# Kernel tuning notes

Measured on AMD Instinct MI355X. Metric: run time of the kernel, lower is better.

Reference implementation:

```python
import jax, jax.numpy as jnp
import numpy as np

N = 20000      # u/v nodes (dst == src, no block sampling)
E = 200000     # edges per direction
EIN = UIN = VIN = EOUT = 64
UOUT = VOUT = 128
NU = UOUT // 2
NV = VOUT // 2
ATT = VIN + EIN  # 128, W_ATTN output / concat dim


def _linear_params(key, din, dout):
    kw, kb = jax.random.split(key)
    s = 1.0 / np.sqrt(din)
    w = jax.random.uniform(kw, (din, dout), jnp.float32, -s, s)
    b = jax.random.uniform(kb, (dout,), jnp.float32, -s, s)
    return w, b


def setup_inputs() -> dict:
    key = jax.random.key(0)
    ks = jax.random.split(key, 20)
    inp = {
        "f_feat": jax.random.normal(ks[0], (E, EIN), jnp.float32),
        "b_feat": jax.random.normal(ks[1], (E, EIN), jnp.float32),
        "u_feat": jax.random.normal(ks[2], (N, UIN), jnp.float32),
        "v_feat": jax.random.normal(ks[3], (N, VIN), jnp.float32),
        "fw_src": jax.random.randint(ks[4], (E,), 0, N, jnp.int32),
        "fw_dst": jax.random.randint(ks[5], (E,), 0, N, jnp.int32),
        "bw_src": jax.random.randint(ks[6], (E,), 0, N, jnp.int32),
        "bw_dst": jax.random.randint(ks[7], (E,), 0, N, jnp.int32),
    }
    names_dims = [("e", EIN, EOUT), ("u", UIN, EOUT), ("v", VIN, EOUT),
                  ("au", UIN, ATT), ("av", VIN, ATT),
                  ("Wu", ATT, NU), ("Wv", ATT, NV),
                  ("Vu", UIN, UOUT - NU), ("Vv", VIN, VOUT - NV)]
    for i, (nm, di, do) in enumerate(names_dims):
        w, b = _linear_params(ks[8 + i], di, do)
        inp["w_" + nm] = w
        inp["b_" + nm] = b
    return inp


def _seg_softmax(x, seg, n):
    # softmax over edges grouped by destination node, per channel
    m = jax.ops.segment_max(x, seg, num_segments=n)       # [n, d]
    e = jnp.exp(x - m[seg])
    s = jax.ops.segment_sum(e, seg, num_segments=n)       # [n, d]
    return e / s[seg]


def reference(f_feat, b_feat, u_feat, v_feat, fw_src, fw_dst, bw_src, bw_dst,
              w_e, b_e, w_u, b_u, w_v, b_v, w_au, b_au, w_av, b_av,
              w_Wu, b_Wu, w_Wv, b_Wv, w_Vu, b_Vu, w_Vv, b_Vv):
    relu = jax.nn.relu
    src_he_u = u_feat @ w_u + b_u                 # [N, EOUT]
    src_he_v = v_feat @ w_v + b_v                 # [N, EOUT]
    dst_he_u = src_he_u                           # dst slice == full set
    dst_he_v = v_feat @ w_u + b_u                 # faithful: original applies u_linear to dst v feats
    fw_he_e = f_feat @ w_e + b_e                  # [E, EOUT]
    bw_he_e = b_feat @ w_e + b_e
    # edge updates (gather-add-activate)
    hf = relu(bw_he_e + dst_he_u[bw_src] + src_he_v[bw_dst])   # [E, EOUT]
    hb = relu(fw_he_e + src_he_u[fw_src] + dst_he_v[fw_dst])
    # per-edge concat features
    h_ve = jnp.concatenate([v_feat[bw_src], b_feat], -1)       # [E, ATT]
    h_ue = jnp.concatenate([u_feat[fw_src], f_feat], -1)       # [E, ATT]
    # attention scores: elementwise edge * gathered node projection
    h_att_u = u_feat @ w_au + b_au                # [N, ATT]
    h_att_v = v_feat @ w_av + b_av
    bw_edotv = h_ve * h_att_u[bw_src]
    fw_edotv = h_ue * h_att_v[fw_src]
    bw_sfm = _seg_softmax(bw_edotv, bw_dst, N)
    fw_sfm = _seg_softmax(fw_edotv, fw_dst, N)
    # weighted segment-sum aggregation
    agg_u = jax.ops.segment_sum(h_ve * bw_sfm, bw_dst, num_segments=N)  # [N, ATT]
    agg_v = jax.ops.segment_sum(h_ue * fw_sfm, fw_dst, num_segments=N)
    h_nu = relu(agg_u @ w_Wu + b_Wu)              # [N, NU]
    h_nv = relu(agg_v @ w_Wv + b_Wv)
    hu = jnp.concatenate([u_feat @ w_Vu + b_Vu, h_nu], -1)     # [N, UOUT]
    hv = jnp.concatenate([v_feat @ w_Vv + b_Vv, h_nv], -1)     # [N, VOUT]
    return (hf, hb, hu, hv)
```

## Files before the change

kernel.cpp:

```cpp
#include <hip/hip_runtime.h>

#define NNODES 20000
#define NEDGES 200000

__global__ __launch_bounds__(256)
void zero_kernel(float4* __restrict__ p, long n4)
{
    long i = (long)blockIdx.x * 256 + threadIdx.x;
    if (i < n4) p[i] = make_float4(0.f, 0.f, 0.f, 0.f);
}

__global__ __launch_bounds__(256)
void hist2_kernel(const int* __restrict__ dst0, const int* __restrict__ dst1,
                  int* __restrict__ deg0, int* __restrict__ deg1, int n)
{
    const int e = blockIdx.x * 256 + threadIdx.x;
    if (e >= n) return;
    if (blockIdx.y == 0) atomicAdd(&deg0[dst0[e]], 1);
    else                 atomicAdd(&deg1[dst1[e]], 1);
}

__global__ __launch_bounds__(1024)
void scan2_kernel(const int* __restrict__ deg0, const int* __restrict__ deg1,
                  int* __restrict__ rp0, int* __restrict__ rp1,
                  int* __restrict__ cur0, int* __restrict__ cur1, int n)
{
    const int* deg = blockIdx.x == 0 ? deg0 : deg1;
    int* rowptr    = blockIdx.x == 0 ? rp0  : rp1;
    int* cursor    = blockIdx.x == 0 ? cur0 : cur1;

    __shared__ int part[1024];
    const int t  = threadIdx.x;
    const int CH = (n + 1023) / 1024;
    const int base = t * CH;

    int s = 0;
    for (int i = 0; i < CH; ++i) {
        int idx = base + i;
        if (idx < n) s += deg[idx];
    }
    part[t] = s;
    __syncthreads();
    for (int off = 1; off < 1024; off <<= 1) {
        int v = 0;
        if (t >= off) v = part[t - off];
        __syncthreads();
        if (t >= off) part[t] += v;
        __syncthreads();
    }
    int run = (t == 0) ? 0 : part[t - 1];
    for (int i = 0; i < CH; ++i) {
        int idx = base + i;
        if (idx < n) {
            int dv = deg[idx];
            rowptr[idx] = run;
            cursor[idx] = run;
            run += dv;
        }
    }
    if (t == 1023) rowptr[n] = part[1023];
}

__global__ __launch_bounds__(256)
void scatter2_kernel(const int* __restrict__ dst0, const int* __restrict__ dst1,
                     int* __restrict__ cur0, int* __restrict__ cur1,
                     int* __restrict__ ei0, int* __restrict__ ei1, int n)
{
    const int e = blockIdx.x * 256 + threadIdx.x;
    if (e >= n) return;
    if (blockIdx.y == 0) { int p = atomicAdd(&cur0[dst0[e]], 1); ei0[p] = e; }
    else                 { int p = atomicAdd(&cur1[dst1[e]], 1); ei1[p] = e; }
}

__global__ __launch_bounds__(128)
void agg3_kernel(const float* __restrict__ fn0, const float* __restrict__ fe0,
                 const float* __restrict__ ha0, const int* __restrict__ src0,
                 const int* __restrict__ ei0,  const int* __restrict__ rp0,
                 float* __restrict__ agg0,
                 const float* __restrict__ fn1, const float* __restrict__ fe1,
                 const float* __restrict__ ha1, const int* __restrict__ src1,
                 const int* __restrict__ ei1,  const int* __restrict__ rp1,
                 float* __restrict__ agg1)
{
    const int y = blockIdx.y;
    const float* __restrict__ feat_node = y == 0 ? fn0 : fn1;
    const float* __restrict__ feat_edge = y == 0 ? fe0 : fe1;
    const float* __restrict__ h_att     = y == 0 ? ha0 : ha1;
    const int*   __restrict__ src       = y == 0 ? src0 : src1;
    const int*   __restrict__ eidx      = y == 0 ? ei0 : ei1;
    const int*   __restrict__ rowptr    = y == 0 ? rp0 : rp1;
    float*       __restrict__ agg       = y == 0 ? agg0 : agg1;

    const int d = blockIdx.x;
    const int c = threadIdx.x;
    const int lo = rowptr[d], hi = rowptr[d + 1];
    const bool low = c < 64;

    __shared__ int se[64];
    __shared__ int ss[64];

    float ssum = 0.f, anum = 0.f;

    for (int base = lo; base < hi; base += 64) {
        const int cnt = min(64, hi - base);
        if (c < cnt) {
            const int e = eidx[base + c];
            se[c] = e;
            ss[c] = src[e];
        }
        __syncthreads();

        int i = 0;
        for (; i + 4 <= cnt; i += 4) {
            float hv[4], at[4];
            #pragma unroll
            for (int j = 0; j < 4; ++j) {
                const int e = se[i + j];
                const int s = ss[i + j];
                hv[j] = low ? feat_node[(long)s * 64 + c]
                            : feat_edge[(long)e * 64 + (c - 64)];
                at[j] = h_att[(long)s * 128 + c];
            }
            #pragma unroll
            for (int j = 0; j < 4; ++j) {
                const float p = __expf(hv[j] * at[j]);
                ssum += p;
                anum += hv[j] * p;
            }
        }
        for (; i < cnt; ++i) {
            const int e = se[i];
            const int s = ss[i];
            const float hvv = low ? feat_node[(long)s * 64 + c]
                                  : feat_edge[(long)e * 64 + (c - 64)];
            const float att = h_att[(long)s * 128 + c];
            const float p = __expf(hvv * att);
            ssum += p;
            anum += hvv * p;
        }
        __syncthreads();
    }
    agg[(long)d * 128 + c] = (hi > lo) ? anum / ssum : 0.f;
}

struct LinArgs {
    const float* x[5];
    const float* W[5];
    const float* bias[5];
    float*       out[5];
    long         ostride[5];
};

template<int DIN, int DOUT, int BLOCK, bool RELU>
__global__ __launch_bounds__(BLOCK)
void lin_batch_kernel(LinArgs a, int nrows)
{
    constexpr int BR  = 16 * BLOCK / DOUT;
    constexpr int BRP = BR + 1;
    constexpr int KV  = DIN / 4;
    constexpr int JT  = DOUT / 4;

    const int y = blockIdx.y;
    const float* __restrict__ x    = a.x[y];
    const float* __restrict__ W    = a.W[y];
    const float* __restrict__ bias = a.bias[y];
    float* __restrict__ out        = a.out[y];
    const long ostride             = a.ostride[y];

    __shared__ float xs[DIN * BRP];
    __shared__ float Ws[DIN * DOUT];

    const int tid  = threadIdx.x;
    const int row0 = blockIdx.x * BR;

    for (int i = tid; i < DIN * DOUT / 4; i += BLOCK)
        ((float4*)Ws)[i] = ((const float4*)W)[i];

    const int kv = tid % KV;
    for (int rr = tid / KV; rr < BR; rr += BLOCK / KV) {
        const int row = row0 + rr;
        float4 v = make_float4(0.f, 0.f, 0.f, 0.f);
        if (row < nrows)
            v = ((const float4*)x)[(long)row * KV + kv];
        xs[(kv * 4 + 0) * BRP + rr] = v.x;
        xs[(kv * 4 + 1) * BRP + rr] = v.y;
        xs[(kv * 4 + 2) * BRP + rr] = v.z;
        xs[(kv * 4 + 3) * BRP + rr] = v.w;
    }
    __syncthreads();

    const int jt = tid % JT;
    const int rt = tid / JT;

    float4 b4 = ((const float4*)bias)[jt];
    float acc[4][4];
    #pragma unroll
    for (int r = 0; r < 4; ++r) {
        acc[r][0] = b4.x; acc[r][1] = b4.y; acc[r][2] = b4.z; acc[r][3] = b4.w;
    }

    #pragma unroll 8
    for (int k = 0; k < DIN; ++k) {
        float4 w = ((const float4*)(Ws + k * DOUT))[jt];
        float xr[4];
        #pragma unroll
        for (int r = 0; r < 4; ++r) xr[r] = xs[k * BRP + rt * 4 + r];
        #pragma unroll
        for (int r = 0; r < 4; ++r) {
            acc[r][0] = fmaf(xr[r], w.x, acc[r][0]);
            acc[r][1] = fmaf(xr[r], w.y, acc[r][1]);
            acc[r][2] = fmaf(xr[r], w.z, acc[r][2]);
            acc[r][3] = fmaf(xr[r], w.w, acc[r][3]);
        }
    }

    #pragma unroll
    for (int r = 0; r < 4; ++r) {
        const int row = row0 + rt * 4 + r;
        if (row >= nrows) continue;
        float4 o = make_float4(acc[r][0], acc[r][1], acc[r][2], acc[r][3]);
        if (RELU) {
            o.x = fmaxf(o.x, 0.f); o.y = fmaxf(o.y, 0.f);
            o.z = fmaxf(o.z, 0.f); o.w = fmaxf(o.w, 0.f);
        }
        *((float4*)(out + (long)row * ostride) + jt) = o;
    }
}

struct EdgeArgs {
    const float* x[2];
    const float* tabA[2];
    const float* tabB[2];
    const int*   idxA[2];
    const int*   idxB[2];
    float*       out[2];
};

__global__ __launch_bounds__(256)
void edge_batch_kernel(EdgeArgs a, const float* __restrict__ W,
                       const float* __restrict__ bias, int nrows)
{
    constexpr int DIN = 64, DOUT = 64, BLOCK = 256;
    constexpr int BR  = 16 * BLOCK / DOUT;
    constexpr int BRP = BR + 1;
    constexpr int KV  = DIN / 4;
    constexpr int JT  = DOUT / 4;

    const int y = blockIdx.y;
    const float* __restrict__ x    = a.x[y];
    const float* __restrict__ tabA = a.tabA[y];
    const float* __restrict__ tabB = a.tabB[y];
    const int* __restrict__ idxA   = a.idxA[y];
    const int* __restrict__ idxB   = a.idxB[y];
    float* __restrict__ out        = a.out[y];

    __shared__ float xs[DIN * BRP];
    __shared__ float Ws[DIN * DOUT];

    const int tid  = threadIdx.x;
    const int row0 = blockIdx.x * BR;

    for (int i = tid; i < DIN * DOUT / 4; i += BLOCK)
        ((float4*)Ws)[i] = ((const float4*)W)[i];

    const int kv = tid % KV;
    for (int rr = tid / KV; rr < BR; rr += BLOCK / KV) {
        const int row = row0 + rr;
        float4 v = make_float4(0.f, 0.f, 0.f, 0.f);
        if (row < nrows)
            v = ((const float4*)x)[(long)row * KV + kv];
        xs[(kv * 4 + 0) * BRP + rr] = v.x;
        xs[(kv * 4 + 1) * BRP + rr] = v.y;
        xs[(kv * 4 + 2) * BRP + rr] = v.z;
        xs[(kv * 4 + 3) * BRP + rr] = v.w;
    }
    __syncthreads();

    const int jt = tid % JT;
    const int rt = tid / JT;

    float4 b4 = ((const float4*)bias)[jt];
    float acc[4][4];
    #pragma unroll
    for (int r = 0; r < 4; ++r) {
        acc[r][0] = b4.x; acc[r][1] = b4.y; acc[r][2] = b4.z; acc[r][3] = b4.w;
    }

    #pragma unroll 8
    for (int k = 0; k < DIN; ++k) {
        float4 w = ((const float4*)(Ws + k * DOUT))[jt];
        float xr[4];
        #pragma unroll
        for (int r = 0; r < 4; ++r) xr[r] = xs[k * BRP + rt * 4 + r];
        #pragma unroll
        for (int r = 0; r < 4; ++r) {
            acc[r][0] = fmaf(xr[r], w.x, acc[r][0]);
            acc[r][1] = fmaf(xr[r], w.y, acc[r][1]);
            acc[r][2] = fmaf(xr[r], w.z, acc[r][2]);
            acc[r][3] = fmaf(xr[r], w.w, acc[r][3]);
        }
    }

    #pragma unroll
    for (int r = 0; r < 4; ++r) {
        const int row = row0 + rt * 4 + r;
        if (row >= nrows) continue;
        const int ia = idxA[row];
        const int ib = idxB[row];
        float4 ga = ((const float4*)(tabA + (long)ia * DOUT))[jt];
        float4 gb = ((const float4*)(tabB + (long)ib * DOUT))[jt];
        float4 o;
        o.x = fmaxf(acc[r][0] + ga.x + gb.x, 0.f);
        o.y = fmaxf(acc[r][1] + ga.y + gb.y, 0.f);
        o.z = fmaxf(acc[r][2] + ga.z + gb.z, 0.f);
        o.w = fmaxf(acc[r][3] + ga.w + gb.w, 0.f);
        *((float4*)(out + (long)row * DOUT) + jt) = o;
    }
}

extern "C" void kernel_launch(void* const* d_in, const int* in_sizes, int n_in,
                              void* d_out, int out_size, void* d_ws, size_t ws_size,
                              hipStream_t stream)
{
    const float* f_feat = (const float*)d_in[0];
    const float* b_feat = (const float*)d_in[1];
    const float* u_feat = (const float*)d_in[2];
    const float* v_feat = (const float*)d_in[3];
    const int* fw_src = (const int*)d_in[4];
    const int* fw_dst = (const int*)d_in[5];
    const int* bw_src = (const int*)d_in[6];
    const int* bw_dst = (const int*)d_in[7];
    const float* w_e  = (const float*)d_in[8];   const float* b_e  = (const float*)d_in[9];
    const float* w_u  = (const float*)d_in[10];  const float* b_u  = (const float*)d_in[11];
    const float* w_v  = (const float*)d_in[12];  const float* b_v  = (const float*)d_in[13];
    const float* w_au = (const float*)d_in[14];  const float* b_au = (const float*)d_in[15];
    const float* w_av = (const float*)d_in[16];  const float* b_av = (const float*)d_in[17];
    const float* w_Wu = (const float*)d_in[18];  const float* b_Wu = (const float*)d_in[19];
    const float* w_Wv = (const float*)d_in[20];  const float* b_Wv = (const float*)d_in[21];
    const float* w_Vu = (const float*)d_in[22];  const float* b_Vu = (const float*)d_in[23];
    const float* w_Vv = (const float*)d_in[24];  const float* b_Vv = (const float*)d_in[25];

    const int N = NNODES, E = NEDGES;

    float* out = (float*)d_out;
    float* hf = out;
    float* hb = hf + (long)E * 64;
    float* hu = hb + (long)E * 64;
    float* hv = hu + (long)N * 128;

    float* h_att_u = hf;
    float* h_att_v = h_att_u + (long)N * 128;

    float* ws = (float*)d_ws;
    float* src_he_u = ws;
    float* src_he_v = src_he_u + (long)N * 64;
    float* dst_he_v = src_he_v + (long)N * 64;
    float* agg_u    = dst_he_v + (long)N * 64;
    float* agg_v    = agg_u    + (long)N * 128;
    int*   ibase    = (int*)(agg_v + (long)N * 128);
    int* deg_b    = ibase;
    int* deg_f    = deg_b + N;
    int* rowptr_b = deg_f + N;
    int* rowptr_f = rowptr_b + (N + 1);
    int* cursor_b = rowptr_f + (N + 1);
    int* cursor_f = cursor_b + N;
    int* eidx_b   = cursor_f + N;
    int* eidx_f   = eidx_b + E;

    const size_t ws_need = (size_t)((long)8960000 + 520002 + 2) * sizeof(float);
    if (ws_size < ws_need) return;

    zero_kernel<<<dim3((2 * N / 4 + 255) / 256), dim3(256), 0, stream>>>(
        (float4*)deg_b, (long)2 * N / 4);

    const int gN64 = (N + 63) / 64;
    const int gN32 = (N + 31) / 32;
    const int gE64 = (E + 63) / 64;
    const int gE   = (E + 255) / 256;

    hist2_kernel<<<dim3(gE, 2), dim3(256), 0, stream>>>(
        bw_dst, fw_dst, deg_b, deg_f, E);
    scan2_kernel<<<dim3(2), dim3(1024), 0, stream>>>(
        deg_b, deg_f, rowptr_b, rowptr_f, cursor_b, cursor_f, N);
    scatter2_kernel<<<dim3(gE, 2), dim3(256), 0, stream>>>(
        bw_dst, fw_dst, cursor_b, cursor_f, eidx_b, eidx_f, E);

    {
        LinArgs a;
        a.x[0]=u_feat; a.W[0]=w_u;  a.bias[0]=b_u;  a.out[0]=src_he_u; a.ostride[0]=64;
        a.x[1]=v_feat; a.W[1]=w_v;  a.bias[1]=b_v;  a.out[1]=src_he_v; a.ostride[1]=64;
        a.x[2]=v_feat; a.W[2]=w_u;  a.bias[2]=b_u;  a.out[2]=dst_he_v; a.ostride[2]=64;
        a.x[3]=u_feat; a.W[3]=w_Vu; a.bias[3]=b_Vu; a.out[3]=hu;       a.ostride[3]=128;
        a.x[4]=v_feat; a.W[4]=w_Vv; a.bias[4]=b_Vv; a.out[4]=hv;       a.ostride[4]=128;
        lin_batch_kernel<64,64,256,false><<<dim3(gN64, 5), dim3(256), 0, stream>>>(a, N);
    }

    {
        LinArgs a = {};
        a.x[0]=u_feat; a.W[0]=w_au; a.bias[0]=b_au; a.out[0]=h_att_u; a.ostride[0]=128;
        a.x[1]=v_feat; a.W[1]=w_av; a.bias[1]=b_av; a.out[1]=h_att_v; a.ostride[1]=128;
        lin_batch_kernel<64,128,256,false><<<dim3(gN32, 2), dim3(256), 0, stream>>>(a, N);
    }

    agg3_kernel<<<dim3(N, 2), dim3(128), 0, stream>>>(
        v_feat, b_feat, h_att_u, bw_src, eidx_b, rowptr_b, agg_u,
        u_feat, f_feat, h_att_v, fw_src, eidx_f, rowptr_f, agg_v);

    {
        LinArgs a = {};
        a.x[0]=agg_u; a.W[0]=w_Wu; a.bias[0]=b_Wu; a.out[0]=hu + 64; a.ostride[0]=128;
        a.x[1]=agg_v; a.W[1]=w_Wv; a.bias[1]=b_Wv; a.out[1]=hv + 64; a.ostride[1]=128;
        lin_batch_kernel<128,64,128,true><<<dim3(gN32, 2), dim3(128), 0, stream>>>(a, N);
    }

    {
        EdgeArgs a;
        a.x[0]=b_feat; a.tabA[0]=src_he_u; a.tabB[0]=src_he_v;
        a.idxA[0]=bw_src; a.idxB[0]=bw_dst; a.out[0]=hf;
        a.x[1]=f_feat; a.tabA[1]=src_he_u; a.tabB[1]=dst_he_v;
        a.idxA[1]=fw_src; a.idxB[1]=fw_dst; a.out[1]=hb;
        edge_batch_kernel<<<dim3(gE64, 2), dim3(256), 0, stream>>>(a, w_e, b_e, E);
    }
}
```

Measured before the change: 476.8 us.

## Map one wavefront per destination node in attention aggregation with shuffles

Restructures the aggregation kernel so each 64-lane wavefront handles one destination node, with each lane covering two channels via float2 loads, and four nodes per 256-thread block. Edge and source indices are broadcast with wave shuffles instead of shared memory, which removes the per-chunk __syncthreads barriers. The aim is to cut synchronisation and block-scheduling overhead and to widen the memory accesses. In exchange each lane does twice the per-edge work, and node degree imbalance within a block can leave waves idle.

```diff
diff --git a/kernel.cpp b/kernel.cpp
--- a/kernel.cpp
+++ b/kernel.cpp
@@ -72,8 +72,8 @@
     else                 { int p = atomicAdd(&cur1[dst1[e]], 1); ei1[p] = e; }
 }
 
-__global__ __launch_bounds__(128)
-void agg3_kernel(const float* __restrict__ fn0, const float* __restrict__ fe0,
+__global__ __launch_bounds__(256)
+void agg4_kernel(const float* __restrict__ fn0, const float* __restrict__ fe0,
                  const float* __restrict__ ha0, const int* __restrict__ src0,
                  const int* __restrict__ ei0,  const int* __restrict__ rp0,
                  float* __restrict__ agg0,
@@ -91,56 +91,43 @@
     const int*   __restrict__ rowptr    = y == 0 ? rp0 : rp1;
     float*       __restrict__ agg       = y == 0 ? agg0 : agg1;
 
-    const int d = blockIdx.x;
-    const int c = threadIdx.x;
+    const int wave = threadIdx.x >> 6;
+    const int lane = threadIdx.x & 63;
+    const int d = blockIdx.x * 4 + wave;
+    if (d >= NNODES) return;
+
     const int lo = rowptr[d], hi = rowptr[d + 1];
-    const bool low = c < 64;
-
-    __shared__ int se[64];
-    __shared__ int ss[64];
-
-    float ssum = 0.f, anum = 0.f;
+    const int c2 = lane * 2;
+    const bool low = lane < 32;
+
+    float s0 = 0.f, s1 = 0.f, a0 = 0.f, a1 = 0.f;
 
     for (int base = lo; base < hi; base += 64) {
         const int cnt = min(64, hi - base);
-        if (c < cnt) {
-            const int e = eidx[base + c];
-            se[c] = e;
-            ss[c] = src[e];
-        }
-        __syncthreads();
-
-        int i = 0;
-        for (; i + 4 <= cnt; i += 4) {
-            float hv[4], at[4];
-            #pragma unroll
-            for (int j = 0; j < 4; ++j) {
-                const int e = se[i + j];
-                const int s = ss[i + j];
-                hv[j] = low ? feat_node[(long)s * 64 + c]
-                            : feat_edge[(long)e * 64 + (c - 64)];
-                at[j] = h_att[(long)s * 128 + c];
-            }
-            #pragma unroll
-            for (int j = 0; j < 4; ++j) {
-                const float p = __expf(hv[j] * at[j]);
-                ssum += p;
-                anum += hv[j] * p;
-            }
-        }
-        for (; i < cnt; ++i) {
-            const int e = se[i];
-            const int s = ss[i];
-            const float hvv = low ? feat_node[(long)s * 64 + c]
-                                  : feat_edge[(long)e * 64 + (c - 64)];
-            const float att = h_att[(long)s * 128 + c];
-            const float p = __expf(hvv * att);
-            ssum += p;
-            anum += hvv * p;
-        }
-        __syncthreads();
-    }
-    agg[(long)d * 128 + c] = (hi > lo) ? anum / ssum : 0.f;
+        int e_l = 0, s_l = 0;
+        if (lane < cnt) {
+            e_l = eidx[base + lane];
+            s_l = src[e_l];
+        }
+        #pragma unroll 4
+        for (int i = 0; i < cnt; ++i) {
+            const int e = __shfl(e_l, i);
+            const int s = __shfl(s_l, i);
+            const float2 at = *(const float2*)(h_att + (long)s * 128 + c2);
+            const float2 hv = low
+                ? *(const float2*)(feat_node + (long)s * 64 + c2)
+                : *(const float2*)(feat_edge + (long)e * 64 + (c2 - 64));
+            const float p0 = __expf(hv.x * at.x);
+            const float p1 = __expf(hv.y * at.y);
+            s0 += p0; s1 += p1;
+            a0 += hv.x * p0; a1 += hv.y * p1;
+        }
+    }
+
+    float2 o;
+    o.x = (hi > lo) ? a0 / s0 : 0.f;
+    o.y = (hi > lo) ? a1 / s1 : 0.f;
+    *(float2*)(agg + (long)d * 128 + c2) = o;
 }
 
 struct LinArgs {
@@ -402,7 +389,7 @@
         lin_batch_kernel<64,128,256,false><<<dim3(gN32, 2), dim3(256), 0, stream>>>(a, N);
     }
 
-    agg3_kernel<<<dim3(N, 2), dim3(128), 0, stream>>>(
+    agg4_kernel<<<dim3((N + 3) / 4, 2), dim3(256), 0, stream>>>(
         v_feat, b_feat, h_att_u, bw_src, eidx_b, rowptr_b, agg_u,
         u_feat, f_feat, h_att_v, fw_src, eidx_f, rowptr_f, agg_v);
 
```

New measurement: 480.8 us. Within noise of the previous version (+0.8%).
